# Kernel optimization log

Measured on AMD Instinct MI355X. Metric: run time of the kernel, lower is better.

The kernel has to match this reference:

```python
import jax, jax.numpy as jnp
import numpy as np

N, H, E, C, V, K = 4096, 256, 128, 32, 64, 20


def setup_inputs() -> dict:
    key = jax.random.key(0)
    ks = jax.random.split(key, 16)
    f = lambda k, s: jax.random.normal(k, s, dtype=jnp.float32)
    return {
        "vec": f(ks[0], (N, H)),
        "inp": f(ks[1], (N, E)),
        "h_prev": f(ks[2], (N, H)),
        "c_prev": f(ks[3], (N, H)),
        "Wlin": f(ks[4], (C, V, H)) * 0.05,
        "blin": f(ks[5], (C, V)) * 0.05,
        "Wec": f(ks[6], (2, H)) * 0.05,
        "bec": f(ks[7], (2,)) * 0.05,
        "Wrel": f(ks[8], (5, H)) * 0.05,
        "brel": f(ks[9], (5,)) * 0.05,
        "W_ih": f(ks[10], (K, 4 * H, E)) * 0.05,
        "b_ih": f(ks[11], (K, 4 * H)) * 0.05,
        "W_hh": f(ks[12], (K, 4 * H, H)) * 0.05,
        "b_hh": f(ks[13], (K, 4 * H)) * 0.05,
        "category": jax.random.randint(ks[14], (N,), 0, C, dtype=jnp.int32),
        "cell_id": jax.random.randint(ks[15], (N,), 0, K, dtype=jnp.int32),
        "true_idx": jax.random.randint(jax.random.fold_in(key, 100), (N,), 0, V, dtype=jnp.int32),
        "ec_idx": jax.random.randint(jax.random.fold_in(key, 101), (N,), 0, 2, dtype=jnp.int32),
        "rel_idx": jax.random.randint(jax.random.fold_in(key, 102), (N,), 0, 5, dtype=jnp.int32),
    }


def _ce(logits, targets):
    # per-row cross entropy (same math as nn.CrossEntropyLoss per example)
    logp = jax.nn.log_softmax(logits, axis=-1)
    return -jnp.take_along_axis(logp, targets[:, None], axis=-1)[:, 0]


def reference(vec, inp, h_prev, c_prev, Wlin, blin, Wec, bec, Wrel, brel,
              W_ih, b_ih, W_hh, b_hh, category, cell_id, true_idx, ec_idx, rel_idx):
    # --- get_log_odds: per-category tiny linear head, selected by category ---
    logits_all = jnp.einsum('nh,cvh->ncv', vec, Wlin) + blin          # [N,C,V]
    logits = jnp.take_along_axis(logits_all, category[:, None, None].astype(jnp.int32), axis=1)[:, 0]  # [N,V]
    logits_ec = vec @ Wec.T + bec                                      # [N,2]
    logits_rel = vec @ Wrel.T + brel                                   # [N,5]

    # --- calculate_loss: CE over valid children + ec + rel ---
    losses = _ce(logits, true_idx) + _ce(logits_ec, ec_idx) + _ce(logits_rel, rel_idx)  # [N]

    # --- get_next: per-child-index LSTMCell, selected by cell_id ---
    gates_all = (jnp.einsum('ne,kge->nkg', inp, W_ih)
                 + jnp.einsum('nh,kgh->nkg', h_prev, W_hh)
                 + b_ih + b_hh)                                        # [N,K,4H]
    gates = jnp.take_along_axis(gates_all, cell_id[:, None, None].astype(jnp.int32), axis=1)[:, 0]  # [N,4H]
    i, f, g, o = jnp.split(gates, 4, axis=-1)                          # torch LSTMCell gate order i,f,g,o
    c_next = jax.nn.sigmoid(f) * c_prev + jax.nn.sigmoid(i) * jnp.tanh(g)
    h_next = jax.nn.sigmoid(o) * jnp.tanh(c_next)

    # pack: [N, 1 + 2H] = loss | h_next | c_next
    return jnp.concatenate([losses[:, None], h_next, c_next], axis=-1)
```

## Files before the change

kernel.cpp:

```cpp
#include <hip/hip_runtime.h>
#include <hip/hip_bf16.h>
#include <math.h>

#define Nn 4096
#define Hdim 256
#define Edim 128
#define Cdim 32
#define Vdim 64
#define Kdim 20
#define G4H 1024
#define OUTS 513

#define SK 512
#define SC 256
#define RK_OFF 64
#define RC_OFF (RK_OFF + Kdim * SK)
#define NLI 18496
#define NSI 18497
#define ITL 18498
#define ITS (ITL + 640)

#define OFF_WF 81920
#define NWF (Kdim * 4 * 12)

#define LSTM_REGION 592
#define LOSS_REGION 320
#define GRID (LSTM_REGION + LOSS_REGION)

typedef short bf16x8 __attribute__((ext_vector_type(8)));
typedef float f32x4 __attribute__((ext_vector_type(4)));
typedef unsigned short u16;

__device__ __forceinline__ float sigmoidf_(float x) { return 1.0f / (1.0f + expf(-x)); }

__device__ __forceinline__ bf16x8 cvt8(float4 f0, float4 f1) {
    bf16x8 r;
    __hip_bfloat16 h;
    h = __float2bfloat16(f0.x); r[0] = *(short*)&h;
    h = __float2bfloat16(f0.y); r[1] = *(short*)&h;
    h = __float2bfloat16(f0.z); r[2] = *(short*)&h;
    h = __float2bfloat16(f0.w); r[3] = *(short*)&h;
    h = __float2bfloat16(f1.x); r[4] = *(short*)&h;
    h = __float2bfloat16(f1.y); r[5] = *(short*)&h;
    h = __float2bfloat16(f1.z); r[6] = *(short*)&h;
    h = __float2bfloat16(f1.w); r[7] = *(short*)&h;
    return r;
}

__device__ __forceinline__ void gl_lds16(const void* g, void* l) {
    __builtin_amdgcn_global_load_lds((const __attribute__((address_space(1))) void*)g,
                                     (__attribute__((address_space(3))) void*)l, 16, 0, 0);
}

__device__ __forceinline__ int swz(int r) { return ((r & 3) << 1) | ((r >> 2) & 1); }

__global__ __launch_bounds__(1024) void k_bucket(const int* __restrict__ cell_id,
                                                 const int* __restrict__ category,
                                                 int* __restrict__ ws) {
    __shared__ int cnt[32];
    __shared__ int off[33];
    int t = threadIdx.x;
    if (t < 32) cnt[t] = 0;
    __syncthreads();
    int i0 = t * 4;
    if (blockIdx.x == 0) {
        int4 v = ((const int4*)cell_id)[t];
        int r;
        r = atomicAdd(&cnt[v.x], 1); if (r < SK) ws[RK_OFF + v.x * SK + r] = i0 + 0;
        r = atomicAdd(&cnt[v.y], 1); if (r < SK) ws[RK_OFF + v.y * SK + r] = i0 + 1;
        r = atomicAdd(&cnt[v.z], 1); if (r < SK) ws[RK_OFF + v.z * SK + r] = i0 + 2;
        r = atomicAdd(&cnt[v.w], 1); if (r < SK) ws[RK_OFF + v.w * SK + r] = i0 + 3;
        __syncthreads();
        if (t == 0) {
            int a = 0;
            for (int kk = 0; kk < Kdim; kk++) { off[kk] = a; a += (min(cnt[kk], SK) + 31) >> 5; }
            ws[NLI] = a * 4;
        }
        __syncthreads();
        if (t < Kdim) {
            int ns = (min(cnt[t], SK) + 31) >> 5;
            int base = off[t];
            for (int s = 0; s < ns; s++)
                for (int hq = 0; hq < 4; hq++)
                    ws[ITL + (base + s) * 4 + hq] = t | (s << 8) | (hq << 16);
        }
        if (t < 32) ws[t] = min(cnt[t], SK);
    } else {
        int4 v = ((const int4*)category)[t];
        int r;
        r = atomicAdd(&cnt[v.x], 1); if (r < SC) ws[RC_OFF + v.x * SC + r] = i0 + 0;
        r = atomicAdd(&cnt[v.y], 1); if (r < SC) ws[RC_OFF + v.y * SC + r] = i0 + 1;
        r = atomicAdd(&cnt[v.z], 1); if (r < SC) ws[RC_OFF + v.z * SC + r] = i0 + 2;
        r = atomicAdd(&cnt[v.w], 1); if (r < SC) ws[RC_OFF + v.w * SC + r] = i0 + 3;
        __syncthreads();
        if (t == 0) {
            int a = 0;
            for (int cc = 0; cc < Cdim; cc++) { off[cc] = a; a += (min(cnt[cc], SC) + 15) >> 4; }
            ws[NSI] = a;
        }
        __syncthreads();
        if (t < Cdim) {
            int ns = (min(cnt[t], SC) + 15) >> 4;
            int base = off[t];
            for (int s = 0; s < ns; s++)
                ws[ITS + base + s] = t | (s << 8);
        }
        if (t < 32) ws[32 + t] = min(cnt[t], SC);
    }
}

__global__ __launch_bounds__(256) void k_wconv(
    const float* __restrict__ W_ih, const float* __restrict__ W_hh,
    int* __restrict__ ws)
{
    u16* WF = (u16*)((char*)ws + OFF_WF);
    int b = blockIdx.x, t = threadIdx.x;
    int l = t & 63, sub = t >> 6;
    int c16 = l & 15, qd = l >> 4;

    int k = b / 48; int r = b - k * 48; int hq = r / 12; int st = r - hq * 12;
    int kk = st * 32 + qd * 8;
    #pragma unroll
    for (int rep = 0; rep < 4; rep++) {
        int idx = sub * 4 + rep;
        int g = idx >> 2, wv = idx & 3;
        int row = g * Hdim + hq * 64 + wv * 16 + c16;
        const float* p = (st < 4)
            ? (W_ih + ((size_t)k * G4H + row) * Edim + kk)
            : (W_hh + ((size_t)k * G4H + row) * Hdim + (kk - Edim));
        float4 lo = *(const float4*)p;
        float4 hi = *(const float4*)(p + 4);
        *(bf16x8*)(WF + ((size_t)(((k * 4 + hq) * 12 + st) * 16 + idx) * 64 + l) * 8) = cvt8(lo, hi);
    }
}

__global__ __launch_bounds__(256, 4) void k_main(
    const float* __restrict__ vec, const float* __restrict__ inp,
    const float* __restrict__ h_prev, const float* __restrict__ c_prev,
    const float* __restrict__ Wlin, const float* __restrict__ blin,
    const float* __restrict__ Wec, const float* __restrict__ bec,
    const float* __restrict__ Wrel, const float* __restrict__ brel,
    const float* __restrict__ b_ih, const float* __restrict__ b_hh,
    const int* __restrict__ true_idx, const int* __restrict__ ec_idx, const int* __restrict__ rel_idx,
    const int* __restrict__ ws,
    float* __restrict__ out)
{
    __shared__ __align__(16) char smem[40960];

    int b = blockIdx.x, t = threadIdx.x;
    int w = t >> 6, l = t & 63;
    int l15 = l & 15, quad = l >> 4;
    int lrow8 = l >> 3, lslot = l & 7;
    int p0 = (quad * 2) ^ swz(l15);

    if (b < LSTM_REGION) {
        if (b >= ws[NLI]) return;
        int item = ws[ITL + b];
        int k = item & 255, s = (item >> 8) & 255, hq = item >> 16;
        int cntk = ws[k];
        int rcount = min(32, cntk - s * 32);
        int reg_row = ws[RK_OFF + k * SK + s * 32 + min(l & 31, rcount - 1)];

        char* Wb = smem;
        float* Xb = (float*)(smem + 32768);
        const char* WFbase = (const char*)ws + OFF_WF + (size_t)((k * 4 + hq) * 12) * 16384;

        int xr = w * 8 + lrow8;
        int xrow = __shfl(reg_row, xr);
        int xg = lslot ^ swz(xr);
        const float* xinp = inp + (size_t)xrow * Edim;
        const float* xhp  = h_prev + (size_t)xrow * Hdim;

        int h = hq * 64 + w * 16 + l15;
        float bs[4];
        #pragma unroll
        for (int g = 0; g < 4; g++)
            bs[g] = b_ih[(size_t)k * G4H + g * Hdim + h] + b_hh[(size_t)k * G4H + g * Hdim + h];
        float cp[2][4];
        #pragma unroll
        for (int m = 0; m < 2; m++)
            #pragma unroll
            for (int reg = 0; reg < 4; reg++) {
                int r = m * 16 + quad * 4 + reg;
                int row = __shfl(reg_row, r);
                cp[m][reg] = c_prev[(size_t)row * Hdim + h];
            }

        f32x4 acc[2][4];
        #pragma unroll
        for (int m = 0; m < 2; m++)
            #pragma unroll
            for (int g = 0; g < 4; g++)
                acc[m][g] = (f32x4){0.f, 0.f, 0.f, 0.f};

        for (int st = 0; st < 6; st++) {
            __syncthreads();
            const char* WFp = WFbase + (size_t)(st * 2) * 16384;
            #pragma unroll
            for (int j = 0; j < 8; j++) {
                int grp = j * 4 + w;
                gl_lds16(WFp + grp * 1024 + l * 16, Wb + grp * 1024);
            }
            #pragma unroll
            for (int half = 0; half < 2; half++) {
                int k0 = (st * 2 + half) * 32;
                const float* Xs = (k0 < Edim) ? xinp + k0 : xhp + (k0 - Edim);
                gl_lds16(Xs + xg * 4, Xb + half * 1024 + (w * 8) * 32);
            }
            __syncthreads();

            #pragma unroll
            for (int kk = 0; kk < 2; kk++) {
                bf16x8 af[2], bfr[4];
                #pragma unroll
                for (int m = 0; m < 2; m++) {
                    int row = m * 16 + l15;
                    float4 lo = *(float4*)(Xb + kk * 1024 + row * 32 + p0 * 4);
                    float4 hi = *(float4*)(Xb + kk * 1024 + row * 32 + (p0 ^ 1) * 4);
                    af[m] = cvt8(lo, hi);
                }
                #pragma unroll
                for (int g = 0; g < 4; g++)
                    bfr[g] = *(bf16x8*)(Wb + kk * 16384 + (g * 4 + w) * 1024 + l * 16);
                #pragma unroll
                for (int m = 0; m < 2; m++)
                    #pragma unroll
                    for (int g = 0; g < 4; g++)
                        acc[m][g] = __builtin_amdgcn_mfma_f32_16x16x32_bf16(af[m], bfr[g], acc[m][g], 0, 0, 0);
            }
        }

        #pragma unroll
        for (int m = 0; m < 2; m++) {
            #pragma unroll
            for (int reg = 0; reg < 4; reg++) {
                int r = m * 16 + quad * 4 + reg;
                int row = __shfl(reg_row, r);
                if (r < rcount) {
                    float iv = acc[m][0][reg] + bs[0];
                    float fv = acc[m][1][reg] + bs[1];
                    float gv = acc[m][2][reg] + bs[2];
                    float ov = acc[m][3][reg] + bs[3];
                    float cn = sigmoidf_(fv) * cp[m][reg] + sigmoidf_(iv) * tanhf(gv);
                    float hn = sigmoidf_(ov) * tanhf(cn);
                    out[(size_t)row * OUTS + 1 + h] = hn;
                    out[(size_t)row * OUTS + 1 + Hdim + h] = cn;
                }
            }
        }
    } else {
        int b2 = b - LSTM_REGION;
        if (b2 >= ws[NSI]) return;
        int item = ws[ITS + b2];
        int c = item & 255, s = item >> 8;
        int cntc = ws[32 + c];
        int rcount = min(16, cntc - s * 16);
        int reg_row = ws[RC_OFF + c * SC + s * 16 + min(l & 15, rcount - 1)];

        float* Wb = (float*)smem;
        float* Vb = (float*)(smem + 10240);
        float* Lg = (float*)(smem + 12288);

        int xr = (w >= 2) ? ((w - 2) * 8 + lrow8) : 0;
        int xrow = __shfl(reg_row, xr);
        int xg = lslot ^ swz(xr);

        f32x4 a0 = (f32x4){0.f, 0.f, 0.f, 0.f};
        f32x4 a1 = (f32x4){0.f, 0.f, 0.f, 0.f};

        for (int st = 0; st < 8; st++) {
            int ko = st * 32;
            __syncthreads();
            for (int n = w; n < 10; n += 4) {
                int r = n * 8 + lrow8;
                int g = lslot ^ swz(r);
                const float* srcW;
                if (r < 64)      srcW = Wlin + ((size_t)c * Vdim + r) * Hdim;
                else if (r < 66) srcW = Wec + (size_t)(r - 64) * Hdim;
                else if (r < 71) srcW = Wrel + (size_t)(r - 66) * Hdim;
                else             srcW = Wlin + (size_t)c * Vdim * Hdim;
                gl_lds16(srcW + ko + g * 4, Wb + n * 8 * 32);
            }
            if (w >= 2)
                gl_lds16(vec + (size_t)xrow * Hdim + ko + xg * 4, Vb + ((w - 2) * 8) * 32);
            __syncthreads();

            bf16x8 af;
            {
                float4 lo = *(float4*)(Vb + l15 * 32 + p0 * 4);
                float4 hi = *(float4*)(Vb + l15 * 32 + (p0 ^ 1) * 4);
                af = cvt8(lo, hi);
            }
            {
                int row = w * 16 + l15;
                float4 lo = *(float4*)(Wb + row * 32 + p0 * 4);
                float4 hi = *(float4*)(Wb + row * 32 + (p0 ^ 1) * 4);
                bf16x8 b0 = cvt8(lo, hi);
                a0 = __builtin_amdgcn_mfma_f32_16x16x32_bf16(af, b0, a0, 0, 0, 0);
            }
            if (w == 3) {
                int row = 64 + l15;
                float4 lo = *(float4*)(Wb + row * 32 + p0 * 4);
                float4 hi = *(float4*)(Wb + row * 32 + (p0 ^ 1) * 4);
                bf16x8 b1 = cvt8(lo, hi);
                a1 = __builtin_amdgcn_mfma_f32_16x16x32_bf16(af, b1, a1, 0, 0, 0);
            }
        }
        __syncthreads();
        {
            int col = w * 16 + l15;
            float bb = blin[c * Vdim + col];
            #pragma unroll
            for (int reg = 0; reg < 4; reg++)
                Lg[(quad * 4 + reg) * 84 + col] = a0[reg] + bb;
            if (w == 3) {
                int col1 = 64 + l15;
                float bb1 = (l15 < 2) ? bec[l15] : ((l15 < 7) ? brel[l15 - 2] : 0.f);
                #pragma unroll
                for (int reg = 0; reg < 4; reg++)
                    Lg[(quad * 4 + reg) * 84 + col1] = a1[reg] + bb1;
            }
        }
        __syncthreads();
        for (int rr = 0; rr < 4; rr++) {
            int r = w * 4 + rr;
            if (r >= rcount) break;
            int orig = __shfl(reg_row, r);
            float lg = Lg[r * 84 + l];
            float mx = lg;
            for (int ss = 32; ss >= 1; ss >>= 1) mx = fmaxf(mx, __shfl_xor(mx, ss));
            float sm = expf(lg - mx);
            for (int ss = 32; ss >= 1; ss >>= 1) sm += __shfl_xor(sm, ss);
            float lt = __shfl(lg, true_idx[orig]);
            float loss = mx + logf(sm) - lt;
            if (l == 0) {
                float l0 = Lg[r * 84 + 64], l1 = Lg[r * 84 + 65];
                float me2 = fmaxf(l0, l1);
                loss += me2 + logf(expf(l0 - me2) + expf(l1 - me2)) - ((ec_idx[orig] == 0) ? l0 : l1);
                float rl[5] = { Lg[r * 84 + 66], Lg[r * 84 + 67], Lg[r * 84 + 68], Lg[r * 84 + 69], Lg[r * 84 + 70] };
                float mr = rl[0];
                #pragma unroll
                for (int i = 1; i < 5; i++) mr = fmaxf(mr, rl[i]);
                float sr = 0.f;
                #pragma unroll
                for (int i = 0; i < 5; i++) sr += expf(rl[i] - mr);
                loss += mr + logf(sr) - rl[rel_idx[orig]];
                out[(size_t)orig * OUTS] = loss;
            }
        }
    }
}

extern "C" void kernel_launch(void* const* d_in, const int* in_sizes, int n_in,
                              void* d_out, int out_size, void* d_ws, size_t ws_size,
                              hipStream_t stream) {
    const float* vec      = (const float*)d_in[0];
    const float* inp      = (const float*)d_in[1];
    const float* h_prev   = (const float*)d_in[2];
    const float* c_prev   = (const float*)d_in[3];
    const float* Wlin     = (const float*)d_in[4];
    const float* blin     = (const float*)d_in[5];
    const float* Wec      = (const float*)d_in[6];
    const float* bec      = (const float*)d_in[7];
    const float* Wrel     = (const float*)d_in[8];
    const float* brel     = (const float*)d_in[9];
    const float* W_ih     = (const float*)d_in[10];
    const float* b_ih     = (const float*)d_in[11];
    const float* W_hh     = (const float*)d_in[12];
    const float* b_hh     = (const float*)d_in[13];
    const int*   category = (const int*)d_in[14];
    const int*   cell_id  = (const int*)d_in[15];
    const int*   true_idx = (const int*)d_in[16];
    const int*   ec_idx   = (const int*)d_in[17];
    const int*   rel_idx  = (const int*)d_in[18];
    float* out = (float*)d_out;
    int* ws = (int*)d_ws;

    k_bucket<<<2, 1024, 0, stream>>>(cell_id, category, ws);
    k_wconv<<<NWF, 256, 0, stream>>>(W_ih, W_hh, ws);
    k_main<<<GRID, 256, 0, stream>>>(
        vec, inp, h_prev, c_prev, Wlin, blin, Wec, bec, Wrel, brel,
        b_ih, b_hh, true_idx, ec_idx, rel_idx, ws, out);
}
```

Baseline: 150.7 us.

## Merge setup kernels, pre-convert loss weights to bf16, remap block order

Fuses the bucketing and LSTM weight-conversion kernels into one setup launch and adds blocks that pre-convert Wlin/Wec/Wrel into a bf16 MFMA-ready fragment layout. The loss path then loads ready-made B fragments instead of converting fp32 weights in every block. It also uses nontemporal stores for the converted weights, reorders LSTM work items so hq is the outer index, and remaps block indices with an XCD-style interleave for locality. This saves a kernel launch and repeated conversion work, at the cost of extra workspace and some added setup work.

```diff
diff --git a/kernel.cpp b/kernel.cpp
--- a/kernel.cpp
+++ b/kernel.cpp
@@ -21,15 +21,21 @@
 #define ITS (ITL + 640)
 
 #define OFF_WF 81920
-#define NWF (Kdim * 4 * 12)
+#define WF_BYTES (Kdim * 4 * 12 * 16384)
+#define OFF_LF (OFF_WF + WF_BYTES)
+#define LF_BYTES (Cdim * 8 * 5 * 1024)
+
+#define NWCONV (Kdim * 4 * 12)
+#define NLCONV (Cdim * 8)
+#define SETUP_GRID (2 + NWCONV + NLCONV)
 
 #define LSTM_REGION 592
 #define LOSS_REGION 320
 #define GRID (LSTM_REGION + LOSS_REGION)
+#define XCHUNK 114
 
 typedef short bf16x8 __attribute__((ext_vector_type(8)));
 typedef float f32x4 __attribute__((ext_vector_type(4)));
-typedef unsigned short u16;
 
 __device__ __forceinline__ float sigmoidf_(float x) { return 1.0f / (1.0f + expf(-x)); }
 
@@ -54,92 +60,116 @@
 
 __device__ __forceinline__ int swz(int r) { return ((r & 3) << 1) | ((r >> 2) & 1); }
 
-__global__ __launch_bounds__(1024) void k_bucket(const int* __restrict__ cell_id,
-                                                 const int* __restrict__ category,
-                                                 int* __restrict__ ws) {
-    __shared__ int cnt[32];
-    __shared__ int off[33];
-    int t = threadIdx.x;
-    if (t < 32) cnt[t] = 0;
-    __syncthreads();
-    int i0 = t * 4;
-    if (blockIdx.x == 0) {
-        int4 v = ((const int4*)cell_id)[t];
-        int r;
-        r = atomicAdd(&cnt[v.x], 1); if (r < SK) ws[RK_OFF + v.x * SK + r] = i0 + 0;
-        r = atomicAdd(&cnt[v.y], 1); if (r < SK) ws[RK_OFF + v.y * SK + r] = i0 + 1;
-        r = atomicAdd(&cnt[v.z], 1); if (r < SK) ws[RK_OFF + v.z * SK + r] = i0 + 2;
-        r = atomicAdd(&cnt[v.w], 1); if (r < SK) ws[RK_OFF + v.w * SK + r] = i0 + 3;
-        __syncthreads();
-        if (t == 0) {
-            int a = 0;
-            for (int kk = 0; kk < Kdim; kk++) { off[kk] = a; a += (min(cnt[kk], SK) + 31) >> 5; }
-            ws[NLI] = a * 4;
-        }
-        __syncthreads();
-        if (t < Kdim) {
-            int ns = (min(cnt[t], SK) + 31) >> 5;
-            int base = off[t];
-            for (int s = 0; s < ns; s++)
-                for (int hq = 0; hq < 4; hq++)
-                    ws[ITL + (base + s) * 4 + hq] = t | (s << 8) | (hq << 16);
-        }
-        if (t < 32) ws[t] = min(cnt[t], SK);
-    } else {
-        int4 v = ((const int4*)category)[t];
-        int r;
-        r = atomicAdd(&cnt[v.x], 1); if (r < SC) ws[RC_OFF + v.x * SC + r] = i0 + 0;
-        r = atomicAdd(&cnt[v.y], 1); if (r < SC) ws[RC_OFF + v.y * SC + r] = i0 + 1;
-        r = atomicAdd(&cnt[v.z], 1); if (r < SC) ws[RC_OFF + v.z * SC + r] = i0 + 2;
-        r = atomicAdd(&cnt[v.w], 1); if (r < SC) ws[RC_OFF + v.w * SC + r] = i0 + 3;
-        __syncthreads();
-        if (t == 0) {
-            int a = 0;
-            for (int cc = 0; cc < Cdim; cc++) { off[cc] = a; a += (min(cnt[cc], SC) + 15) >> 4; }
-            ws[NSI] = a;
-        }
-        __syncthreads();
-        if (t < Cdim) {
-            int ns = (min(cnt[t], SC) + 15) >> 4;
-            int base = off[t];
-            for (int s = 0; s < ns; s++)
-                ws[ITS + base + s] = t | (s << 8);
-        }
-        if (t < 32) ws[32 + t] = min(cnt[t], SC);
-    }
-}
-
-__global__ __launch_bounds__(256) void k_wconv(
+__global__ __launch_bounds__(256) void k_setup(
+    const int* __restrict__ cell_id, const int* __restrict__ category,
     const float* __restrict__ W_ih, const float* __restrict__ W_hh,
+    const float* __restrict__ Wlin, const float* __restrict__ Wec, const float* __restrict__ Wrel,
     int* __restrict__ ws)
 {
-    u16* WF = (u16*)((char*)ws + OFF_WF);
     int b = blockIdx.x, t = threadIdx.x;
-    int l = t & 63, sub = t >> 6;
-    int c16 = l & 15, qd = l >> 4;
-
-    int k = b / 48; int r = b - k * 48; int hq = r / 12; int st = r - hq * 12;
-    int kk = st * 32 + qd * 8;
-    #pragma unroll
-    for (int rep = 0; rep < 4; rep++) {
-        int idx = sub * 4 + rep;
-        int g = idx >> 2, wv = idx & 3;
-        int row = g * Hdim + hq * 64 + wv * 16 + c16;
-        const float* p = (st < 4)
-            ? (W_ih + ((size_t)k * G4H + row) * Edim + kk)
-            : (W_hh + ((size_t)k * G4H + row) * Hdim + (kk - Edim));
-        float4 lo = *(const float4*)p;
-        float4 hi = *(const float4*)(p + 4);
-        *(bf16x8*)(WF + ((size_t)(((k * 4 + hq) * 12 + st) * 16 + idx) * 64 + l) * 8) = cvt8(lo, hi);
+
+    if (b < 2) {
+        __shared__ int cnt[32];
+        __shared__ int off[32];
+        if (t < 32) cnt[t] = 0;
+        __syncthreads();
+        const int* key = (b == 0) ? cell_id : category;
+        int cap = (b == 0) ? SK : SC;
+        int roff = (b == 0) ? RK_OFF : RC_OFF;
+        int stride = cap;
+        #pragma unroll
+        for (int j = 0; j < 4; j++) {
+            int4 v = ((const int4*)key)[t * 4 + j];
+            int i0 = t * 16 + j * 4;
+            int r;
+            r = atomicAdd(&cnt[v.x], 1); if (r < cap) ws[roff + v.x * stride + r] = i0 + 0;
+            r = atomicAdd(&cnt[v.y], 1); if (r < cap) ws[roff + v.y * stride + r] = i0 + 1;
+            r = atomicAdd(&cnt[v.z], 1); if (r < cap) ws[roff + v.z * stride + r] = i0 + 2;
+            r = atomicAdd(&cnt[v.w], 1); if (r < cap) ws[roff + v.w * stride + r] = i0 + 3;
+        }
+        __syncthreads();
+        if (b == 0) {
+            if (t == 0) {
+                int a = 0;
+                for (int kk = 0; kk < Kdim; kk++) { off[kk] = a; a += (min(cnt[kk], SK) + 31) >> 5; }
+                ws[NLI] = a * 4;
+            }
+            __syncthreads();
+            if (t < Kdim) {
+                int ns = (min(cnt[t], SK) + 31) >> 5;
+                int base = off[t] * 4;
+                for (int hq = 0; hq < 4; hq++)
+                    for (int s = 0; s < ns; s++)
+                        ws[ITL + base + hq * ns + s] = t | (s << 8) | (hq << 16);
+            }
+            if (t < 32) ws[t] = min(cnt[t], SK);
+        } else {
+            if (t == 0) {
+                int a = 0;
+                for (int cc = 0; cc < Cdim; cc++) { off[cc] = a; a += (min(cnt[cc], SC) + 15) >> 4; }
+                ws[NSI] = a;
+            }
+            __syncthreads();
+            if (t < Cdim) {
+                int ns = (min(cnt[t], SC) + 15) >> 4;
+                int base = off[t];
+                for (int s = 0; s < ns; s++)
+                    ws[ITS + base + s] = t | (s << 8);
+            }
+            if (t < 32) ws[32 + t] = min(cnt[t], SC);
+        }
+    } else if (b < 2 + NWCONV) {
+        int b2 = b - 2;
+        int l = t & 63, sub = t >> 6;
+        int c16 = l & 15, qd = l >> 4;
+        int k = b2 / 48; int r = b2 - k * 48; int hq = r / 12; int st = r - hq * 12;
+        int kk = st * 32 + qd * 8;
+        char* WF = (char*)ws + OFF_WF;
+        #pragma unroll
+        for (int rep = 0; rep < 4; rep++) {
+            int idx = sub * 4 + rep;
+            int g = idx >> 2, wv = idx & 3;
+            int row = g * Hdim + hq * 64 + wv * 16 + c16;
+            const float* p = (st < 4)
+                ? (W_ih + ((size_t)k * G4H + row) * Edim + kk)
+                : (W_hh + ((size_t)k * G4H + row) * Hdim + (kk - Edim));
+            float4 lo = *(const float4*)p;
+            float4 hi = *(const float4*)(p + 4);
+            bf16x8 v = cvt8(lo, hi);
+            __builtin_nontemporal_store(v,
+                (bf16x8*)(WF + (size_t)((((k * 4 + hq) * 12 + st) * 16 + idx) * 64 + l) * 16));
+        }
+    } else {
+        int b3 = b - 2 - NWCONV;
+        int l = t & 63, sub = t >> 6;
+        int c16 = l & 15, qd = l >> 4;
+        int c = b3 >> 3; int st = b3 & 7;
+        int kk = st * 32 + qd * 8;
+        char* LF = (char*)ws + OFF_LF;
+        for (int wg = sub; wg < 5; wg += 4) {
+            int lr = wg * 16 + c16;
+            bf16x8 v;
+            if (lr < 71) {
+                const float* p;
+                if (lr < 64)      p = Wlin + ((size_t)c * Vdim + lr) * Hdim + kk;
+                else if (lr < 66) p = Wec + (size_t)(lr - 64) * Hdim + kk;
+                else              p = Wrel + (size_t)(lr - 66) * Hdim + kk;
+                float4 lo = *(const float4*)p;
+                float4 hi = *(const float4*)(p + 4);
+                v = cvt8(lo, hi);
+            } else {
+                v = (bf16x8){0, 0, 0, 0, 0, 0, 0, 0};
+            }
+            __builtin_nontemporal_store(v,
+                (bf16x8*)(LF + (size_t)(((c * 8 + st) * 5 + wg) * 64 + l) * 16));
+        }
     }
 }
 
 __global__ __launch_bounds__(256, 4) void k_main(
     const float* __restrict__ vec, const float* __restrict__ inp,
     const float* __restrict__ h_prev, const float* __restrict__ c_prev,
-    const float* __restrict__ Wlin, const float* __restrict__ blin,
-    const float* __restrict__ Wec, const float* __restrict__ bec,
-    const float* __restrict__ Wrel, const float* __restrict__ brel,
+    const float* __restrict__ blin, const float* __restrict__ bec, const float* __restrict__ brel,
     const float* __restrict__ b_ih, const float* __restrict__ b_hh,
     const int* __restrict__ true_idx, const int* __restrict__ ec_idx, const int* __restrict__ rel_idx,
     const int* __restrict__ ws,
@@ -147,15 +177,17 @@
 {
     __shared__ __align__(16) char smem[40960];
 
-    int b = blockIdx.x, t = threadIdx.x;
+    int t = threadIdx.x;
     int w = t >> 6, l = t & 63;
     int l15 = l & 15, quad = l >> 4;
     int lrow8 = l >> 3, lslot = l & 7;
     int p0 = (quad * 2) ^ swz(l15);
 
-    if (b < LSTM_REGION) {
-        if (b >= ws[NLI]) return;
-        int item = ws[ITL + b];
+    int work = (blockIdx.x & 7) * XCHUNK + (blockIdx.x >> 3);
+
+    if (work < LSTM_REGION) {
+        if (work >= ws[NLI]) return;
+        int item = ws[ITL + work];
         int k = item & 255, s = (item >> 8) & 255, hq = item >> 16;
         int cntk = ws[k];
         int rcount = min(32, cntk - s * 32);
@@ -249,17 +281,18 @@
             }
         }
     } else {
-        int b2 = b - LSTM_REGION;
-        if (b2 >= ws[NSI]) return;
-        int item = ws[ITS + b2];
+        int work2 = work - LSTM_REGION;
+        if (work2 >= ws[NSI]) return;
+        int item = ws[ITS + work2];
         int c = item & 255, s = item >> 8;
         int cntc = ws[32 + c];
         int rcount = min(16, cntc - s * 16);
         int reg_row = ws[RC_OFF + c * SC + s * 16 + min(l & 15, rcount - 1)];
 
-        float* Wb = (float*)smem;
-        float* Vb = (float*)(smem + 10240);
-        float* Lg = (float*)(smem + 12288);
+        char* Wb = smem;
+        float* Vb = (float*)(smem + 5120);
+        float* Lg = (float*)(smem + 7168);
+        const char* LFbase = (const char*)ws + OFF_LF + (size_t)(c * 8) * 5120;
 
         int xr = (w >= 2) ? ((w - 2) * 8 + lrow8) : 0;
         int xrow = __shfl(reg_row, xr);
@@ -269,20 +302,12 @@
         f32x4 a1 = (f32x4){0.f, 0.f, 0.f, 0.f};
 
         for (int st = 0; st < 8; st++) {
-            int ko = st * 32;
-            __syncthreads();
-            for (int n = w; n < 10; n += 4) {
-                int r = n * 8 + lrow8;
-                int g = lslot ^ swz(r);
-                const float* srcW;
-                if (r < 64)      srcW = Wlin + ((size_t)c * Vdim + r) * Hdim;
-                else if (r < 66) srcW = Wec + (size_t)(r - 64) * Hdim;
-                else if (r < 71) srcW = Wrel + (size_t)(r - 66) * Hdim;
-                else             srcW = Wlin + (size_t)c * Vdim * Hdim;
-                gl_lds16(srcW + ko + g * 4, Wb + n * 8 * 32);
-            }
+            __syncthreads();
+            const char* LFp = LFbase + (size_t)st * 5120;
+            for (int n = w; n < 5; n += 4)
+                gl_lds16(LFp + n * 1024 + l * 16, Wb + n * 1024);
             if (w >= 2)
-                gl_lds16(vec + (size_t)xrow * Hdim + ko + xg * 4, Vb + ((w - 2) * 8) * 32);
+                gl_lds16(vec + (size_t)xrow * Hdim + st * 32 + xg * 4, Vb + ((w - 2) * 8) * 32);
             __syncthreads();
 
             bf16x8 af;
@@ -292,17 +317,11 @@
                 af = cvt8(lo, hi);
             }
             {
-                int row = w * 16 + l15;
-                float4 lo = *(float4*)(Wb + row * 32 + p0 * 4);
-                float4 hi = *(float4*)(Wb + row * 32 + (p0 ^ 1) * 4);
-                bf16x8 b0 = cvt8(lo, hi);
+                bf16x8 b0 = *(bf16x8*)(Wb + w * 1024 + l * 16);
                 a0 = __builtin_amdgcn_mfma_f32_16x16x32_bf16(af, b0, a0, 0, 0, 0);
             }
             if (w == 3) {
-                int row = 64 + l15;
-                float4 lo = *(float4*)(Wb + row * 32 + p0 * 4);
-                float4 hi = *(float4*)(Wb + row * 32 + (p0 ^ 1) * 4);
-                bf16x8 b1 = cvt8(lo, hi);
+                bf16x8 b1 = *(bf16x8*)(Wb + 4 * 1024 + l * 16);
                 a1 = __builtin_amdgcn_mfma_f32_16x16x32_bf16(af, b1, a1, 0, 0, 0);
             }
         }
@@ -376,9 +395,9 @@
     float* out = (float*)d_out;
     int* ws = (int*)d_ws;
 
-    k_bucket<<<2, 1024, 0, stream>>>(cell_id, category, ws);
-    k_wconv<<<NWF, 256, 0, stream>>>(W_ih, W_hh, ws);
+    k_setup<<<SETUP_GRID, 256, 0, stream>>>(cell_id, category, W_ih, W_hh,
+                                            Wlin, Wec, Wrel, ws);
     k_main<<<GRID, 256, 0, stream>>>(
-        vec, inp, h_prev, c_prev, Wlin, blin, Wec, bec, Wrel, brel,
+        vec, inp, h_prev, c_prev, blin, bec, brel,
         b_ih, b_hh, true_idx, ec_idx, rel_idx, ws, out);
 }
```

Result: no change. 148.5 us (-1.5%).
